# Optimization experiments

Measured on AMD Instinct MI355X. Metric: run time of the kernel, lower is better.

Reference implementation:

```python
import jax, jax.numpy as jnp
import numpy as np

B, T, V, E, H = 512, 256, 50000, 512, 1024


def setup_inputs() -> dict:
    key = jax.random.key(0)
    ks = jax.random.split(key, 10)
    s_in = 1.0 / np.sqrt(E + H)  # torch Linear default init scale
    s_fc = 1.0 / np.sqrt(H)
    return {
        "x": jax.random.randint(ks[0], (B, T), 0, V),
        "emb": jax.random.normal(ks[1], (V, E), dtype=jnp.float32),
        "W_r": jax.random.uniform(ks[2], (E + H, H), jnp.float32, -s_in, s_in),
        "b_r": jax.random.uniform(ks[3], (H,), jnp.float32, -s_in, s_in),
        "W_z": jax.random.uniform(ks[4], (E + H, H), jnp.float32, -s_in, s_in),
        "b_z": jax.random.uniform(ks[5], (H,), jnp.float32, -s_in, s_in),
        "W_c": jax.random.uniform(ks[6], (E + H, H), jnp.float32, -s_in, s_in),
        "b_c": jax.random.uniform(ks[7], (H,), jnp.float32, -s_in, s_in),
        "W_fc": jax.random.uniform(ks[8], (H, 1), jnp.float32, -s_fc, s_fc),
        "b_fc": jax.random.uniform(ks[9], (1,), jnp.float32, -s_fc, s_fc),
    }


def reference(x, emb, W_r, b_r, W_z, b_z, W_c, b_c, W_fc, b_fc):
    embedded = emb[x]                      # [B, T, E]
    xs = jnp.swapaxes(embedded, 0, 1)      # [T, B, E] for scan over time
    h0 = jnp.zeros((x.shape[0], H), dtype=emb.dtype)

    # fuse r and z gates: same input, one GEMM
    W_rz = jnp.concatenate([W_r, W_z], axis=1)   # [E+H, 2H]
    b_rz = jnp.concatenate([b_r, b_z], axis=0)   # [2H]

    def step(h, xt):
        combined = jnp.concatenate([xt, h], axis=1)          # [B, E+H]
        rz = jax.nn.sigmoid(combined @ W_rz + b_rz)          # [B, 2H]
        r, z = rz[:, :H], rz[:, H:]
        cc = jnp.concatenate([xt, r * h], axis=1)            # [B, E+H]
        h_tilde = jnp.tanh(cc @ W_c + b_c)                   # [B, H]
        h_new = (1.0 - z) * h + z * h_tilde
        return h_new, None

    h_T, _ = jax.lax.scan(step, h0, xs)
    return jax.nn.sigmoid(h_T @ W_fc + b_fc)                 # [B, 1]
```

## Files before the change

kernel.cpp:

```cpp
#include <hip/hip_runtime.h>
#include <hip/hip_bf16.h>

#define B_ 512
#define T_ 256
#define E_ 512
#define H_ 1024
#define K_ 1536

typedef __attribute__((ext_vector_type(4))) float f32x4;
typedef __attribute__((ext_vector_type(8))) short s16x8;
typedef __attribute__((ext_vector_type(4))) unsigned int u32x4;
typedef __attribute__((ext_vector_type(2))) unsigned int u32x2;

typedef unsigned int u32_g __attribute__((address_space(1)));
typedef unsigned int u32_l __attribute__((address_space(3)));

static __device__ __forceinline__ void gload16(const void* g, void* l) {
    __builtin_amdgcn_global_load_lds((const u32_g*)g, (u32_l*)l, 16, 0, 0);
}

static __device__ __forceinline__ short f2b(float f) {
    union { float f; unsigned u; } v; v.f = f;
    unsigned r = v.u + 0x7FFFu + ((v.u >> 16) & 1u);
    return (short)(r >> 16);
}
static __device__ __forceinline__ float bf2f(short s) {
    union { unsigned u; float f; } v; v.u = ((unsigned)(unsigned short)s) << 16;
    return v.f;
}
static __device__ __forceinline__ float sigmoidf_(float v) {
    return 1.f / (1.f + expf(-v));
}

#define WAITV(n) asm volatile("s_waitcnt vmcnt(" #n ")" ::: "memory")
#define WAITL    asm volatile("s_waitcnt lgkmcnt(0)" ::: "memory")
#define SB0 __builtin_amdgcn_sched_barrier(0)

static __device__ __forceinline__ u32x4 load16sc(const short* p) {
    u32x4 r;
    asm volatile("global_load_dwordx4 %0, %1, off sc1" : "=v"(r) : "v"(p));
    return r;
}
static __device__ __forceinline__ u32x2 load8sc(const short* p) {
    u32x2 r;
    asm volatile("global_load_dwordx2 %0, %1, off sc1" : "=v"(r) : "v"(p));
    return r;
}
static __device__ __forceinline__ void store2sc(const short* p, unsigned v) {
    asm volatile("global_store_short %0, %1, off sc1" :: "v"(p), "v"(v) : "memory");
}

#define FR(buf, row, k) \
    (*(const s16x8*)&(buf)[(row) * 128 + ((((k) >> 3) ^ ((row) & 7)) << 3)])


__global__ __launch_bounds__(256) void prep_fast(
    const float* __restrict__ W_r, const float* __restrict__ W_z,
    const float* __restrict__ W_c, const float* __restrict__ emb,
    short* __restrict__ We, short* __restrict__ Wh, short* __restrict__ embb,
    float* __restrict__ hbuf, short* __restrict__ hb16, unsigned* __restrict__ flags)
{
    const int NW = 3072 * 1536;
    const int NE = 50048 * 512;
    const int NH = 512 * 1024;
    const int NF = 8192;
    const int total = NW + NE + NH + NF;
    for (int idx = blockIdx.x * 256 + threadIdx.x; idx < total; idx += gridDim.x * 256) {
        if (idx < NW) {
            int n = idx / 1536, k = idx - n * 1536;
            const float* W = n < 1024 ? W_r : (n < 2048 ? W_z : W_c);
            float v = W[(size_t)k * 1024 + (n & 1023)];
            if (k < 512) We[(size_t)n * 512 + k] = f2b(v);
            else         Wh[(size_t)n * 1024 + (k - 512)] = f2b(v);
        } else if (idx < NW + NE) {
            int e = idx - NW; int row = e >> 9;
            embb[e] = row < 50000 ? f2b(emb[e]) : (short)0;
        } else if (idx < NW + NE + NH) {
            int h = idx - NW - NE;
            hbuf[h] = 0.f; hb16[h] = 0;
        } else {
            flags[idx - NW - NE - NH] = 0u;
        }
    }
}

__global__ __launch_bounds__(256) void vproj_gemm(
    const short* __restrict__ embb, const short* __restrict__ We,
    short* __restrict__ vp)
{
    __shared__ short As[128 * 64];
    __shared__ short Bs[128 * 64];
    const int tid = threadIdx.x, lane = tid & 63, w = tid >> 6;
    const int wm = (w >> 1) * 64, wn = (w & 1) * 64;
    const int m0 = blockIdx.x * 128, n0 = blockIdx.y * 128;
    f32x4 acc[4][4] = {};
    for (int kc = 0; kc < 8; ++kc) {
        int k0 = kc * 64;
        #pragma unroll
        for (int ii = 0; ii < 4; ++ii) {
            int i = w * 4 + ii;
            int row = i * 8 + (lane >> 3), kk = (lane & 7) * 8;
            gload16(embb + (size_t)(m0 + row) * 512 + k0 + kk, As + i * 512);
            gload16(We   + (size_t)(n0 + row) * 512 + k0 + kk, Bs + i * 512);
        }
        __syncthreads();
        #pragma unroll
        for (int kk = 0; kk < 64; kk += 32) {
            s16x8 a[4], b[4];
            #pragma unroll
            for (int f = 0; f < 4; ++f) {
                a[f] = *(const s16x8*)&As[(wm + f * 16 + (lane & 15)) * 64 + kk + (lane >> 4) * 8];
                b[f] = *(const s16x8*)&Bs[(wn + f * 16 + (lane & 15)) * 64 + kk + (lane >> 4) * 8];
            }
            #pragma unroll
            for (int fm = 0; fm < 4; ++fm)
            #pragma unroll
            for (int fn = 0; fn < 4; ++fn)
                acc[fm][fn] = __builtin_amdgcn_mfma_f32_16x16x32_bf16(a[fm], b[fn], acc[fm][fn], 0, 0, 0);
        }
        __syncthreads();
    }
    #pragma unroll
    for (int fm = 0; fm < 4; ++fm)
    #pragma unroll
    for (int fn = 0; fn < 4; ++fn)
    #pragma unroll
    for (int r = 0; r < 4; ++r) {
        int row = m0 + wm + fm * 16 + (lane >> 4) * 4 + r;
        int col = n0 + wn + fn * 16 + (lane & 15);
        vp[(size_t)row * 3072 + col] = f2b(acc[fm][fn][r]);
    }
}

static __device__ __forceinline__ void groupbar2(unsigned* gf, int member, unsigned gen) {
    WAITV(0);
    __syncthreads();
    if (threadIdx.x == 0) {
        __hip_atomic_store(&gf[member * 16], gen,
                           __ATOMIC_RELAXED, __HIP_MEMORY_SCOPE_AGENT);
    }
    if (threadIdx.x < 32) {
        unsigned v = __hip_atomic_load(&gf[threadIdx.x * 16],
                                       __ATOMIC_RELAXED, __HIP_MEMORY_SCOPE_AGENT);
        int spins = 0;
        while (v < gen) {
            __builtin_amdgcn_s_sleep(1);
            v = __hip_atomic_load(&gf[threadIdx.x * 16],
                                  __ATOMIC_RELAXED, __HIP_MEMORY_SCOPE_AGENT);
            if (++spins > (1 << 18)) break;
        }
    }
    __syncthreads();
}

template<int PH>
static __device__ __forceinline__ void phaseX(
    const short* __restrict__ Ab,
    const short* __restrict__ Wh,
    const short* __restrict__ vp, const int* __restrict__ xidxL,
    int g, int n, int t,
    short* AL, short* BL, short* XpL, float* zL, short* hL,
    const float* br, const float* bz, float bc,
    short* __restrict__ rh16, short* __restrict__ hb16,
    float* __restrict__ hbuf, f32x4& h_reg)
{
    const int tid = threadIdx.x, lane = tid & 63, w = tid >> 6;
    const int wm = (w >> 1) * 16;
    const int wn = (PH == 1) ? (w & 1) * 32 : (w & 1) * 16;
    constexpr int BROWS = (PH == 1) ? 64 : 32;
    constexpr int BJ    = (PH == 1) ? 4 : 2;
    constexpr int BUFSZ = BROWS * 128;

    u32x4 xp4; u32x2 xp2;
    if constexpr (PH == 1) {
        int row = tid >> 3, part = tid & 7;
        int col = (part < 4) ? (n * 32 + part * 8) : (1024 + n * 32 + (part - 4) * 8);
        xp4 = load16sc(vp + (size_t)xidxL[row] * 3072 + col);
    } else {
        int row = tid >> 3, part = tid & 7;
        xp2 = load8sc(vp + (size_t)xidxL[row] * 3072 + 2048 + n * 32 + part * 4);
    }

    auto issueA = [&](int c, u32x4* dst) {
        #pragma unroll
        for (int j = 0; j < 2; ++j) {
            int sid = j * 256 + tid, row = sid >> 4, sg = (sid & 15) ^ (row & 7);
            dst[j] = load16sc(Ab + (size_t)row * 1024 + c * 128 + sg * 8);
        }
    };
    auto issueB = [&](int c, int buf) {
        #pragma unroll
        for (int j = 0; j < BJ; ++j) {
            int sid = j * 256 + tid, row = sid >> 4, sg = (sid & 15) ^ (row & 7);
            int grow;
            if constexpr (PH == 1) grow = (row < 32) ? (n * 32 + row) : (1024 + n * 32 + row - 32);
            else                   grow = 2048 + n * 32 + row;
            gload16(Wh + (size_t)grow * 1024 + c * 128 + sg * 8,
                    BL + buf * BUFSZ + (j * 256 + w * 64) * 8);
        }
    };
    auto writeA = [&](int buf, const u32x4* src) {
        #pragma unroll
        for (int j = 0; j < 2; ++j) {
            int sid = j * 256 + tid;
            *(u32x4*)&AL[buf * 4096 + sid * 8] = src[j];
        }
    };

    u32x4 ra[2][2];
    issueA(0, ra[0]); issueB(0, 0);
    issueA(1, ra[1]); issueB(1, 1);
    if constexpr (PH == 1) { WAITV(6); } else { WAITV(4); }
    SB0;
    writeA(0, ra[0]);
    {
        int row = tid >> 3, part = tid & 7;
        if constexpr (PH == 1) {
            int dst = (part < 4) ? part * 8 : (32 + (part - 4) * 8);
            *(u32x4*)&XpL[row * 64 + dst] = xp4;
        } else {
            *(u32x2*)&XpL[row * 32 + part * 4] = xp2;
        }
    }
    WAITL;
    __builtin_amdgcn_s_barrier();
    SB0;

    f32x4 acc[2] = {};
    #pragma unroll
    for (int kc = 0; kc < 8; ++kc) {
        if (kc < 6) { issueA(kc + 2, ra[kc & 1]); issueB(kc + 2, (kc + 2) % 3); }
        const short* Ac = AL + (kc & 1) * 4096;
        const short* Bc = BL + (kc % 3) * BUFSZ;
        __builtin_amdgcn_s_setprio(1);
        #pragma unroll
        for (int ks = 0; ks < 4; ++ks) {
            const int kf = ks * 32 + (lane >> 4) * 8;
            s16x8 a = FR(Ac, wm + (lane & 15), kf);
            if constexpr (PH == 1) {
                s16x8 b0 = FR(Bc, wn + (lane & 15), kf);
                s16x8 b1 = FR(Bc, wn + 16 + (lane & 15), kf);
                acc[0] = __builtin_amdgcn_mfma_f32_16x16x32_bf16(a, b0, acc[0], 0, 0, 0);
                acc[1] = __builtin_amdgcn_mfma_f32_16x16x32_bf16(a, b1, acc[1], 0, 0, 0);
            } else {
                s16x8 b0 = FR(Bc, wn + (lane & 15), kf);
                acc[0] = __builtin_amdgcn_mfma_f32_16x16x32_bf16(a, b0, acc[0], 0, 0, 0);
            }
        }
        __builtin_amdgcn_s_setprio(0);
        if (kc < 7) {
            if (kc < 6) { if constexpr (PH == 1) { WAITV(6); } else { WAITV(4); } }
            else        { WAITV(0); }
            SB0;
            writeA((kc + 1) & 1, ra[(kc + 1) & 1]);
            WAITL;
            __builtin_amdgcn_s_barrier();
            SB0;
        }
    }

    const int rl0 = wm + (lane >> 4) * 4;
    if constexpr (PH == 1) {
        if ((w & 1) == 0) {
            #pragma unroll
            for (int fn = 0; fn < 2; ++fn) {
                int cl = fn * 16 + (lane & 15);
                #pragma unroll
                for (int ri = 0; ri < 4; ++ri) {
                    int rl = rl0 + ri;
                    float v = acc[fn][ri] + bf2f(XpL[rl * 64 + cl]) + br[fn];
                    float rr = sigmoidf_(v);
                    float hv = bf2f(hL[rl * 32 + cl]);
                    store2sc(rh16 + (size_t)(g * 32 + rl) * 1024 + n * 32 + cl,
                             (unsigned)(unsigned short)f2b(rr * hv));
                }
            }
        } else {
            #pragma unroll
            for (int fn = 0; fn < 2; ++fn) {
                int zc = fn * 16 + (lane & 15);
                #pragma unroll
                for (int ri = 0; ri < 4; ++ri) {
                    int rl = rl0 + ri;
                    float v = acc[fn][ri] + bf2f(XpL[rl * 64 + 32 + zc]) + bz[fn];
                    zL[rl * 32 + zc] = sigmoidf_(v);
                }
            }
        }
    } else {
        int cl2 = wn + (lane & 15);
        #pragma unroll
        for (int ri = 0; ri < 4; ++ri) {
            int rl = rl0 + ri;
            float v = acc[0][ri] + bf2f(XpL[rl * 32 + cl2]) + bc;
            float c = tanhf(v);
            float zv = zL[rl * 32 + cl2];
            float h = h_reg[ri];
            float hn = h + zv * (c - h);
            h_reg[ri] = hn;
            short hb = f2b(hn);
            store2sc(hb16 + (size_t)(g * 32 + rl) * 1024 + n * 32 + cl2,
                     (unsigned)(unsigned short)hb);
            hL[rl * 32 + cl2] = hb;
            if (t == T_ - 1)
                hbuf[(size_t)(g * 32 + rl) * 1024 + n * 32 + cl2] = hn;
        }
    }
}

__global__ __launch_bounds__(256, 2) void gru_persistent(
    const int* __restrict__ x, const short* __restrict__ Wh,
    const short* __restrict__ vp,
    const float* __restrict__ b_r, const float* __restrict__ b_z,
    const float* __restrict__ b_c,
    float* __restrict__ hbuf, short* __restrict__ hb16,
    short* __restrict__ rh16, unsigned* __restrict__ flags)
{
    __shared__ short AL[2 * 4096];
    __shared__ short BL[3 * 8192];
    __shared__ short XpL[2048];
    __shared__ float zL[1024];
    __shared__ short hL[1024];
    __shared__ int xidxL[32];

    const int bid = blockIdx.x;
    const int g = bid >> 5, n = bid & 31;
    unsigned* gf = flags + g * 512;

    const int tid = threadIdx.x, lane = tid & 63, w = tid >> 6;
    const int wm = (w >> 1) * 16, wn2 = (w & 1) * 16;

    float br[2], bz[2], bc;
    #pragma unroll
    for (int fn = 0; fn < 2; ++fn) {
        br[fn] = b_r[n * 32 + fn * 16 + (lane & 15)];
        bz[fn] = b_z[n * 32 + fn * 16 + (lane & 15)];
    }
    bc = b_c[n * 32 + wn2 + (lane & 15)];

    f32x4 h_reg = {0.f, 0.f, 0.f, 0.f};
    #pragma unroll
    for (int ri = 0; ri < 4; ++ri)
        hL[(wm + (lane >> 4) * 4 + ri) * 32 + wn2 + (lane & 15)] = 0;

    for (int t = 0; t < T_; ++t) {
        if (tid < 32) xidxL[tid] = x[(g * 32 + tid) * T_ + t];
        __syncthreads();
        phaseX<1>(hb16 + (size_t)(g * 32) * 1024, Wh, vp, xidxL, g, n, t,
                  AL, BL, XpL, zL, hL, br, bz, bc, rh16, hb16, hbuf, h_reg);
        groupbar2(gf, n, 2 * t + 1);
        phaseX<2>(rh16 + (size_t)(g * 32) * 1024, Wh, vp, xidxL, g, n, t,
                  AL, BL, XpL, zL, hL, br, bz, bc, rh16, hb16, hbuf, h_reg);
        if (t < T_ - 1) groupbar2(gf, n, 2 * t + 2);
    }
}

__global__ __launch_bounds__(256) void fc_kernel(
    const float* __restrict__ h, const float* __restrict__ Wfc,
    const float* __restrict__ bfc, float* __restrict__ out)
{
    int gw   = (blockIdx.x * 256 + threadIdx.x) >> 6;
    int lane = threadIdx.x & 63;
    if (gw >= B_) return;
    float s = 0.f;
    for (int j = lane; j < H_; j += 64) s += h[(size_t)gw * H_ + j] * Wfc[j];
    #pragma unroll
    for (int off = 32; off; off >>= 1) s += __shfl_down(s, off);
    if (lane == 0) out[gw] = sigmoidf_(s + bfc[0]);
}

__global__ __launch_bounds__(256) void prep_fb(
    const float* __restrict__ W_r, const float* __restrict__ W_z,
    const float* __restrict__ W_c,
    short* __restrict__ Wt_rz, short* __restrict__ Wt_c,
    float* __restrict__ hbuf, short* __restrict__ hbf16)
{
    const int PER = H_ * K_;
    int idx = blockIdx.x * 256 + threadIdx.x;
    if (idx < PER * 3) {
        int mm = idx / PER, rem = idx - mm * PER;
        int n = rem / K_, k = rem - n * K_;
        if (mm == 0)      Wt_rz[(size_t)n * K_ + k]        = f2b(W_r[(size_t)k * H_ + n]);
        else if (mm == 1) Wt_rz[(size_t)(H_ + n) * K_ + k] = f2b(W_z[(size_t)k * H_ + n]);
        else              Wt_c[(size_t)n * K_ + k]         = f2b(W_c[(size_t)k * H_ + n]);
    }
    if (idx < B_ * H_) { hbuf[idx] = 0.f; hbf16[idx] = 0; }
}

template<int MODE>
__global__ __launch_bounds__(256) void gru_gemm(
    const int* __restrict__ x, const float* __restrict__ emb,
    const short* __restrict__ Wt, const short* __restrict__ hpart,
    const float* __restrict__ bias0, const float* __restrict__ bias1,
    const float* __restrict__ hbuf, float* __restrict__ zbuf,
    short* __restrict__ rh_out, float* __restrict__ h_out,
    short* __restrict__ hb_out, int t)
{
    __shared__ short As2[64][72];
    __shared__ short Bs2[64][72];
    __shared__ int xidx2[64];
    const int tid = threadIdx.x;
    const int bm = blockIdx.x, bn = blockIdx.y;
    if (tid < 64) xidx2[tid] = x[(bm * 64 + tid) * T_ + t];
    f32x4 acc[2][2] = {};
    const int m  = tid >> 2;
    const int ks = (tid & 3) * 16;
    const int w  = tid >> 6, lane = tid & 63;
    const int wm = (w >> 1) * 32, wn = (w & 1) * 32;
    const int lr = lane & 15, lk = (lane >> 4) * 8;
    __syncthreads();
    for (int kt = 0; kt < 24; ++kt) {
        const int k0 = kt * 64;
        if (k0 < E_) {
            const int row = xidx2[m];
            const float4* src = (const float4*)&emb[(size_t)row * E_ + k0 + ks];
            short tmp[16];
            #pragma unroll
            for (int v = 0; v < 4; ++v) {
                float4 f = src[v];
                tmp[v*4+0] = f2b(f.x); tmp[v*4+1] = f2b(f.y);
                tmp[v*4+2] = f2b(f.z); tmp[v*4+3] = f2b(f.w);
            }
            *(s16x8*)&As2[m][ks]     = *(const s16x8*)&tmp[0];
            *(s16x8*)&As2[m][ks + 8] = *(const s16x8*)&tmp[8];
        } else {
            const s16x8* src = (const s16x8*)&hpart[(size_t)(bm*64 + m) * H_ + (k0 - E_ + ks)];
            *(s16x8*)&As2[m][ks]     = src[0];
            *(s16x8*)&As2[m][ks + 8] = src[1];
        }
        {
            const s16x8* src = (const s16x8*)&Wt[(size_t)(bn*64 + m) * K_ + k0 + ks];
            *(s16x8*)&Bs2[m][ks]     = src[0];
            *(s16x8*)&Bs2[m][ks + 8] = src[1];
        }
        __syncthreads();
        #pragma unroll
        for (int kk = 0; kk < 64; kk += 32) {
            s16x8 a0 = *(const s16x8*)&As2[wm      + lr][kk + lk];
            s16x8 a1 = *(const s16x8*)&As2[wm + 16 + lr][kk + lk];
            s16x8 b0 = *(const s16x8*)&Bs2[wn      + lr][kk + lk];
            s16x8 b1 = *(const s16x8*)&Bs2[wn + 16 + lr][kk + lk];
            acc[0][0] = __builtin_amdgcn_mfma_f32_16x16x32_bf16(a0, b0, acc[0][0], 0, 0, 0);
            acc[0][1] = __builtin_amdgcn_mfma_f32_16x16x32_bf16(a0, b1, acc[0][1], 0, 0, 0);
            acc[1][0] = __builtin_amdgcn_mfma_f32_16x16x32_bf16(a1, b0, acc[1][0], 0, 0, 0);
            acc[1][1] = __builtin_amdgcn_mfma_f32_16x16x32_bf16(a1, b1, acc[1][1], 0, 0, 0);
        }
        __syncthreads();
    }
    #pragma unroll
    for (int fm = 0; fm < 2; ++fm)
    #pragma unroll
    for (int fn = 0; fn < 2; ++fn)
    #pragma unroll
    for (int r = 0; r < 4; ++r) {
        const int row = bm * 64 + wm + fm * 16 + ((lane >> 4) * 4 + r);
        const int n   = bn * 64 + wn + fn * 16 + (lane & 15);
        float v = acc[fm][fn][r];
        if (MODE == 0) {
            if (n < H_) {
                float rr = sigmoidf_(v + bias0[n]);
                size_t idx = (size_t)row * H_ + n;
                rh_out[idx] = f2b(rr * hbuf[idx]);
            } else {
                int nz = n - H_;
                zbuf[(size_t)row * H_ + nz] = sigmoidf_(v + bias1[nz]);
            }
        } else {
            float ht = tanhf(v + bias0[n]);
            size_t idx = (size_t)row * H_ + n;
            float h = hbuf[idx], z = zbuf[idx];
            float hn = (1.f - z) * h + z * ht;
            h_out[idx]  = hn;
            hb_out[idx] = f2b(hn);
        }
    }
}

extern "C" void kernel_launch(void* const* d_in, const int* in_sizes, int n_in,
                              void* d_out, int out_size, void* d_ws, size_t ws_size,
                              hipStream_t stream) {
    const int*   x    = (const int*)  d_in[0];
    const float* emb  = (const float*)d_in[1];
    const float* W_r  = (const float*)d_in[2];
    const float* b_r  = (const float*)d_in[3];
    const float* W_z  = (const float*)d_in[4];
    const float* b_z  = (const float*)d_in[5];
    const float* W_c  = (const float*)d_in[6];
    const float* b_c  = (const float*)d_in[7];
    const float* W_fc = (const float*)d_in[8];
    const float* b_fc = (const float*)d_in[9];

    char* ws = (char*)d_ws;
    const size_t NEED = 374489088ULL;

    if (ws_size >= NEED) {
        short*    We    = (short*)(ws);
        short*    Wh    = (short*)(ws + 3145728);
        short*    embb  = (short*)(ws + 9437184);
        short*    vp    = (short*)(ws + 60686336);
        float*    hbuf  = (float*)(ws + 368181248);
        short*    hb16  = (short*)(ws + 370278400);
        short*    rh16  = (short*)(ws + 371326976);
        unsigned* flags = (unsigned*)(ws + 372375552);

        prep_fast<<<2048, 256, 0, stream>>>(W_r, W_z, W_c, emb, We, Wh, embb, hbuf, hb16, flags);
        vproj_gemm<<<dim3(391, 24), 256, 0, stream>>>(embb, We, vp);
        gru_persistent<<<512, 256, 0, stream>>>(x, Wh, vp, b_r, b_z, b_c,
                                                hbuf, hb16, rh16, flags);
        fc_kernel<<<128, 256, 0, stream>>>(hbuf, W_fc, b_fc, (float*)d_out);
    } else {
        short* Wt_rz  = (short*)(ws);
        short* Wt_c   = (short*)(ws + 6291456);
        float* hbuf   = (float*)(ws + 9437184);
        short* hbf16  = (short*)(ws + 11534336);
        short* rhbf16 = (short*)(ws + 12582912);
        float* zbuf   = (float*)(ws + 13631488);

        prep_fb<<<18432, 256, 0, stream>>>(W_r, W_z, W_c, Wt_rz, Wt_c, hbuf, hbf16);
        for (int t = 0; t < T_; ++t) {
            gru_gemm<0><<<dim3(8, 32), 256, 0, stream>>>(
                x, emb, Wt_rz, hbf16, b_r, b_z, hbuf, zbuf, rhbf16, nullptr, nullptr, t);
            gru_gemm<1><<<dim3(8, 16), 256, 0, stream>>>(
                x, emb, Wt_c, rhbf16, b_c, nullptr, hbuf, zbuf, nullptr, hbuf, hbf16, t);
        }
        fc_kernel<<<128, 256, 0, stream>>>(hbuf, W_fc, b_fc, (float*)d_out);
    }
}
```

Before: 5.381 ms.

## Load A tiles directly to LDS with triple buffering, double-buffer weights

The activation (A) tiles now go straight from global memory into LDS through global_load_lds with the sc bit set, instead of being staged through registers and written with ds_write. The buffering is swapped: A gets three LDS stages and is prefetched two chunks ahead, while the weight (B) tiles drop to two stages and are prefetched one chunk ahead. This removes the register staging, the LDS write and one lgkmcnt wait per chunk. In exchange the weight loads have less lead time, and the wait counts are re-tuned by hand, so a wrong count could create a race.

```diff
diff --git a/kernel.cpp b/kernel.cpp
--- a/kernel.cpp
+++ b/kernel.cpp
@@ -17,6 +17,9 @@
 
 static __device__ __forceinline__ void gload16(const void* g, void* l) {
     __builtin_amdgcn_global_load_lds((const u32_g*)g, (u32_l*)l, 16, 0, 0);
+}
+static __device__ __forceinline__ void gload16sc(const void* g, void* l) {
+    __builtin_amdgcn_global_load_lds((const u32_g*)g, (u32_l*)l, 16, 0, 16);
 }
 
 static __device__ __forceinline__ short f2b(float f) {
@@ -181,11 +184,12 @@
         xp2 = load8sc(vp + (size_t)xidxL[row] * 3072 + 2048 + n * 32 + part * 4);
     }
 
-    auto issueA = [&](int c, u32x4* dst) {
+    auto issueA = [&](int c, int buf) {
         #pragma unroll
         for (int j = 0; j < 2; ++j) {
             int sid = j * 256 + tid, row = sid >> 4, sg = (sid & 15) ^ (row & 7);
-            dst[j] = load16sc(Ab + (size_t)row * 1024 + c * 128 + sg * 8);
+            gload16sc(Ab + (size_t)row * 1024 + c * 128 + sg * 8,
+                      AL + buf * 4096 + (j * 256 + w * 64) * 8);
         }
     };
     auto issueB = [&](int c, int buf) {
@@ -199,20 +203,12 @@
                     BL + buf * BUFSZ + (j * 256 + w * 64) * 8);
         }
     };
-    auto writeA = [&](int buf, const u32x4* src) {
-        #pragma unroll
-        for (int j = 0; j < 2; ++j) {
-            int sid = j * 256 + tid;
-            *(u32x4*)&AL[buf * 4096 + sid * 8] = src[j];
-        }
-    };
-
-    u32x4 ra[2][2];
-    issueA(0, ra[0]); issueB(0, 0);
-    issueA(1, ra[1]); issueB(1, 1);
-    if constexpr (PH == 1) { WAITV(6); } else { WAITV(4); }
+
+    issueB(0, 0);
+    issueA(0, 0);
+    issueA(1, 1);
+    WAITV(2);
     SB0;
-    writeA(0, ra[0]);
     {
         int row = tid >> 3, part = tid & 7;
         if constexpr (PH == 1) {
@@ -229,9 +225,10 @@
     f32x4 acc[2] = {};
     #pragma unroll
     for (int kc = 0; kc < 8; ++kc) {
-        if (kc < 6) { issueA(kc + 2, ra[kc & 1]); issueB(kc + 2, (kc + 2) % 3); }
-        const short* Ac = AL + (kc & 1) * 4096;
-        const short* Bc = BL + (kc % 3) * BUFSZ;
+        if (kc < 7) issueB(kc + 1, (kc + 1) & 1);
+        if (kc < 6) issueA(kc + 2, (kc + 2) % 3);
+        const short* Ac = AL + (kc % 3) * 4096;
+        const short* Bc = BL + (kc & 1) * BUFSZ;
         __builtin_amdgcn_s_setprio(1);
         #pragma unroll
         for (int ks = 0; ks < 4; ++ks) {
@@ -249,11 +246,8 @@
         }
         __builtin_amdgcn_s_setprio(0);
         if (kc < 7) {
-            if (kc < 6) { if constexpr (PH == 1) { WAITV(6); } else { WAITV(4); } }
-            else        { WAITV(0); }
+            if (kc < 6) { WAITV(2); } else { WAITV(0); }
             SB0;
-            writeA((kc + 1) & 1, ra[(kc + 1) & 1]);
-            WAITL;
             __builtin_amdgcn_s_barrier();
             SB0;
         }
@@ -316,8 +310,8 @@
     float* __restrict__ hbuf, short* __restrict__ hb16,
     short* __restrict__ rh16, unsigned* __restrict__ flags)
 {
-    __shared__ short AL[2 * 4096];
-    __shared__ short BL[3 * 8192];
+    __shared__ short AL[3 * 4096];
+    __shared__ short BL[2 * 8192];
     __shared__ short XpL[2048];
     __shared__ float zL[1024];
     __shared__ short hL[1024];
```

After: 5.273 ms. -2.0%, faster.
